# Optimization experiments

Hardware: AMD Instinct MI355X
Metric: run time of the kernel (lower is better)

The kernel has to match this reference:

```python
import jax, jax.numpy as jnp
import numpy as np

N_NODES = 50000
N_EDGES = 800000
D_IN = 128
D_OUT = 64


def setup_inputs() -> dict:
    key = jax.random.key(0)
    k_x, k_src, k_dst, k_val, k_w = jax.random.split(key, 5)
    x = jax.random.normal(k_x, (N_NODES, D_IN), dtype=jnp.float32)
    edge_src = jax.random.randint(k_src, (N_EDGES,), 0, N_NODES, dtype=jnp.int32)
    edge_dst = jnp.sort(jax.random.randint(k_dst, (N_EDGES,), 0, N_NODES, dtype=jnp.int32))
    edge_vals = jax.random.uniform(k_val, (N_EDGES,), dtype=jnp.float32)
    # Xavier-uniform init for weight, zeros for bias (matches reset_parameters)
    limit = float(np.sqrt(6.0 / (D_IN + D_OUT)))
    weight = jax.random.uniform(k_w, (D_IN, D_OUT), minval=-limit, maxval=limit, dtype=jnp.float32)
    bias = jnp.zeros((D_OUT,), dtype=jnp.float32)
    return {"x": x, "edge_src": edge_src, "edge_dst": edge_dst,
            "edge_vals": edge_vals, "weight": weight, "bias": bias}


def reference(x, edge_src, edge_dst, edge_vals, weight, bias):
    # Dense projection: [N, D_in] @ [D_in, D_out] -> [N, D_out]
    h = x @ weight
    # Sparse adjacency matmul (torch.spmm): out[i] = sum_{(j->i) in E} A_val * h[j]
    msgs = edge_vals[:, None] * h[edge_src]          # [E, D_out]
    agg = jax.ops.segment_sum(msgs, edge_dst, num_segments=N_NODES)  # [N, D_out]
    return agg + bias
```

## Files before the change

kernel.cpp:

```cpp
#include <hip/hip_runtime.h>

#define D_IN  128
#define D_OUT 64

__global__ __launch_bounds__(256, 4) void gemm_h_kernel(
    const float* __restrict__ x, const float* __restrict__ w,
    float* __restrict__ h, int n_nodes)
{
    __shared__ float Xs[64 * 132];
    __shared__ float Ws[128 * 64];

    const int t   = threadIdx.x;
    const int tx  = t & 15;
    const int ty  = t >> 4;
    const int node0 = blockIdx.x * 64;

    #pragma unroll
    for (int j = 0; j < 8; ++j) {
        int idx = j * 256 + t;
        int k   = idx >> 4;
        int c   = idx & 15;
        float4 v = *(const float4*)&w[k * D_OUT + c * 4];
        *(float4*)&Ws[k * 64 + c * 4] = v;
    }
    #pragma unroll
    for (int j = 0; j < 8; ++j) {
        int idx = j * 256 + t;
        int r   = idx >> 5;
        int c   = idx & 31;
        int gn  = node0 + r;
        float4 v = make_float4(0.f, 0.f, 0.f, 0.f);
        if (gn < n_nodes) v = *(const float4*)&x[(size_t)gn * D_IN + c * 4];
        *(float4*)&Xs[r * 132 + c * 4] = v;
    }
    __syncthreads();

    float4 acc[4];
    #pragma unroll
    for (int i = 0; i < 4; ++i) acc[i] = make_float4(0.f, 0.f, 0.f, 0.f);

    const int d0 = tx * 4;
    const int n0 = ty * 4;

    #pragma unroll 2
    for (int k = 0; k < D_IN; k += 4) {
        float4 xa[4], wb[4];
        #pragma unroll
        for (int i = 0; i < 4; ++i)
            xa[i] = *(const float4*)&Xs[(n0 + i) * 132 + k];
        #pragma unroll
        for (int r = 0; r < 4; ++r)
            wb[r] = *(const float4*)&Ws[(k + r) * 64 + d0];
        #pragma unroll
        for (int i = 0; i < 4; ++i) {
            acc[i].x = fmaf(xa[i].x, wb[0].x, acc[i].x);
            acc[i].y = fmaf(xa[i].x, wb[0].y, acc[i].y);
            acc[i].z = fmaf(xa[i].x, wb[0].z, acc[i].z);
            acc[i].w = fmaf(xa[i].x, wb[0].w, acc[i].w);
            acc[i].x = fmaf(xa[i].y, wb[1].x, acc[i].x);
            acc[i].y = fmaf(xa[i].y, wb[1].y, acc[i].y);
            acc[i].z = fmaf(xa[i].y, wb[1].z, acc[i].z);
            acc[i].w = fmaf(xa[i].y, wb[1].w, acc[i].w);
            acc[i].x = fmaf(xa[i].z, wb[2].x, acc[i].x);
            acc[i].y = fmaf(xa[i].z, wb[2].y, acc[i].y);
            acc[i].z = fmaf(xa[i].z, wb[2].z, acc[i].z);
            acc[i].w = fmaf(xa[i].z, wb[2].w, acc[i].w);
            acc[i].x = fmaf(xa[i].w, wb[3].x, acc[i].x);
            acc[i].y = fmaf(xa[i].w, wb[3].y, acc[i].y);
            acc[i].z = fmaf(xa[i].w, wb[3].z, acc[i].z);
            acc[i].w = fmaf(xa[i].w, wb[3].w, acc[i].w);
        }
    }

    #pragma unroll
    for (int i = 0; i < 4; ++i) {
        int gn = node0 + n0 + i;
        if (gn < n_nodes)
            *(float4*)&h[(size_t)gn * D_OUT + d0] = acc[i];
    }
}

__global__ __launch_bounds__(256) void build_row_ptr_kernel(
    const int* __restrict__ dst, int* __restrict__ row_ptr, int n_edges, int n_nodes)
{
    int e = blockIdx.x * blockDim.x + threadIdx.x;
    if (e >= n_edges) return;
    int d1 = dst[e];
    int d0 = (e == 0) ? -1 : dst[e - 1];
    for (int j = d0 + 1; j <= d1; ++j) row_ptr[j] = e;
    if (e == n_edges - 1) {
        for (int j = d1 + 1; j <= n_nodes; ++j) row_ptr[j] = n_edges;
    }
}

__global__ __launch_bounds__(256) void aggregate_kernel(
    const float4* __restrict__ h4, const int* __restrict__ src,
    const float* __restrict__ vals, const int* __restrict__ row_ptr,
    const float* __restrict__ bias, float* __restrict__ out, int n_nodes)
{
    int wave = (blockIdx.x * blockDim.x + threadIdx.x) >> 6;
    int lane = threadIdx.x & 63;
    if (wave >= n_nodes) return;
    int sub = lane >> 4;
    int d4  = lane & 15;

    int b = row_ptr[wave];
    int e = row_ptr[wave + 1];

    float4 acc = make_float4(0.f, 0.f, 0.f, 0.f);
    int k = b + sub;
    for (; k + 4 < e; k += 8) {
        int   s0 = src[k];     float v0 = vals[k];
        int   s1 = src[k + 4]; float v1 = vals[k + 4];
        float4 h0 = h4[(size_t)s0 * 16 + d4];
        float4 h1 = h4[(size_t)s1 * 16 + d4];
        acc.x = fmaf(v0, h0.x, acc.x);
        acc.y = fmaf(v0, h0.y, acc.y);
        acc.z = fmaf(v0, h0.z, acc.z);
        acc.w = fmaf(v0, h0.w, acc.w);
        acc.x = fmaf(v1, h1.x, acc.x);
        acc.y = fmaf(v1, h1.y, acc.y);
        acc.z = fmaf(v1, h1.z, acc.z);
        acc.w = fmaf(v1, h1.w, acc.w);
    }
    if (k < e) {
        int   s0 = src[k];
        float v0 = vals[k];
        float4 h0 = h4[(size_t)s0 * 16 + d4];
        acc.x = fmaf(v0, h0.x, acc.x);
        acc.y = fmaf(v0, h0.y, acc.y);
        acc.z = fmaf(v0, h0.z, acc.z);
        acc.w = fmaf(v0, h0.w, acc.w);
    }

    #pragma unroll
    for (int off = 16; off < 64; off <<= 1) {
        acc.x += __shfl_xor(acc.x, off, 64);
        acc.y += __shfl_xor(acc.y, off, 64);
        acc.z += __shfl_xor(acc.z, off, 64);
        acc.w += __shfl_xor(acc.w, off, 64);
    }

    if (sub == 0) {
        float4 bb = *(const float4*)&bias[d4 * 4];
        float4 o;
        o.x = acc.x + bb.x;
        o.y = acc.y + bb.y;
        o.z = acc.z + bb.z;
        o.w = acc.w + bb.w;
        *(float4*)&out[(size_t)wave * D_OUT + d4 * 4] = o;
    }
}

extern "C" void kernel_launch(void* const* d_in, const int* in_sizes, int n_in,
                              void* d_out, int out_size, void* d_ws, size_t ws_size,
                              hipStream_t stream)
{
    const float* x         = (const float*)d_in[0];
    const int*   edge_src  = (const int*)  d_in[1];
    const int*   edge_dst  = (const int*)  d_in[2];
    const float* edge_vals = (const float*)d_in[3];
    const float* weight    = (const float*)d_in[4];
    const float* bias      = (const float*)d_in[5];
    float*       out       = (float*)d_out;

    const int n_nodes = in_sizes[0] / D_IN;
    const int n_edges = in_sizes[1];

    float* h       = (float*)d_ws;
    int*   row_ptr = (int*)((char*)d_ws + (size_t)n_nodes * D_OUT * sizeof(float));

    {
        dim3 grid((n_nodes + 63) / 64), block(256);
        hipLaunchKernelGGL(gemm_h_kernel, grid, block, 0, stream, x, weight, h, n_nodes);
    }
    {
        dim3 grid((n_edges + 255) / 256), block(256);
        hipLaunchKernelGGL(build_row_ptr_kernel, grid, block, 0, stream,
                           edge_dst, row_ptr, n_edges, n_nodes);
    }
    {
        dim3 grid((n_nodes + 3) / 4), block(256);
        hipLaunchKernelGGL(aggregate_kernel, grid, block, 0, stream,
                           (const float4*)h, edge_src, edge_vals, row_ptr, bias, out, n_nodes);
    }
}
```

Baseline: 129.6 us.

## Merge row-pointer build into GEMM launch and deepen aggregation unroll

Folds the CSR row-pointer construction into the GEMM kernel as extra blocks in the same grid, removing one kernel launch and letting both independent jobs run concurrently. The aggregation loop is unrolled to 16 edges per iteration with two accumulators to keep more gathers in flight. The output is written with nontemporal stores. The extra blocks share the GEMM's large shared-memory footprint, which can limit their occupancy, and the wider unroll raises register use.

```diff
diff --git a/kernel.cpp b/kernel.cpp
--- a/kernel.cpp
+++ b/kernel.cpp
@@ -3,12 +3,34 @@
 #define D_IN  128
 #define D_OUT 64
 
-__global__ __launch_bounds__(256, 4) void gemm_h_kernel(
+typedef float nfloat4 __attribute__((ext_vector_type(4)));
+
+__global__ __launch_bounds__(256, 4) void gemm_rowptr_kernel(
     const float* __restrict__ x, const float* __restrict__ w,
-    float* __restrict__ h, int n_nodes)
+    float* __restrict__ h, int n_nodes,
+    const int* __restrict__ dst, int* __restrict__ row_ptr, int n_edges,
+    int gemm_blocks)
 {
     __shared__ float Xs[64 * 132];
     __shared__ float Ws[128 * 64];
+
+    if ((int)blockIdx.x >= gemm_blocks) {
+        int rb   = (int)blockIdx.x - gemm_blocks;
+        int base = rb * 1024 + (int)threadIdx.x;
+        #pragma unroll
+        for (int j = 0; j < 4; ++j) {
+            int e = base + j * 256;
+            if (e < n_edges) {
+                int d1 = dst[e];
+                int d0 = (e == 0) ? -1 : dst[e - 1];
+                for (int q = d0 + 1; q <= d1; ++q) row_ptr[q] = e;
+                if (e == n_edges - 1) {
+                    for (int q = d1 + 1; q <= n_nodes; ++q) row_ptr[q] = n_edges;
+                }
+            }
+        }
+        return;
+    }
 
     const int t   = threadIdx.x;
     const int tx  = t & 15;
@@ -80,19 +102,6 @@
     }
 }
 
-__global__ __launch_bounds__(256) void build_row_ptr_kernel(
-    const int* __restrict__ dst, int* __restrict__ row_ptr, int n_edges, int n_nodes)
-{
-    int e = blockIdx.x * blockDim.x + threadIdx.x;
-    if (e >= n_edges) return;
-    int d1 = dst[e];
-    int d0 = (e == 0) ? -1 : dst[e - 1];
-    for (int j = d0 + 1; j <= d1; ++j) row_ptr[j] = e;
-    if (e == n_edges - 1) {
-        for (int j = d1 + 1; j <= n_nodes; ++j) row_ptr[j] = n_edges;
-    }
-}
-
 __global__ __launch_bounds__(256) void aggregate_kernel(
     const float4* __restrict__ h4, const int* __restrict__ src,
     const float* __restrict__ vals, const int* __restrict__ row_ptr,
@@ -107,31 +116,67 @@
     int b = row_ptr[wave];
     int e = row_ptr[wave + 1];
 
-    float4 acc = make_float4(0.f, 0.f, 0.f, 0.f);
+    float4 bb = *(const float4*)&bias[d4 * 4];
+
+    float4 acc0 = make_float4(0.f, 0.f, 0.f, 0.f);
+    float4 acc1 = make_float4(0.f, 0.f, 0.f, 0.f);
+
     int k = b + sub;
+    for (; k + 12 < e; k += 16) {
+        int   s0 = src[k];      int   s1 = src[k + 4];
+        int   s2 = src[k + 8];  int   s3 = src[k + 12];
+        float v0 = vals[k];     float v1 = vals[k + 4];
+        float v2 = vals[k + 8]; float v3 = vals[k + 12];
+        float4 h0 = h4[(size_t)s0 * 16 + d4];
+        float4 h1 = h4[(size_t)s1 * 16 + d4];
+        float4 h2 = h4[(size_t)s2 * 16 + d4];
+        float4 h3 = h4[(size_t)s3 * 16 + d4];
+        acc0.x = fmaf(v0, h0.x, acc0.x);
+        acc0.y = fmaf(v0, h0.y, acc0.y);
+        acc0.z = fmaf(v0, h0.z, acc0.z);
+        acc0.w = fmaf(v0, h0.w, acc0.w);
+        acc1.x = fmaf(v1, h1.x, acc1.x);
+        acc1.y = fmaf(v1, h1.y, acc1.y);
+        acc1.z = fmaf(v1, h1.z, acc1.z);
+        acc1.w = fmaf(v1, h1.w, acc1.w);
+        acc0.x = fmaf(v2, h2.x, acc0.x);
+        acc0.y = fmaf(v2, h2.y, acc0.y);
+        acc0.z = fmaf(v2, h2.z, acc0.z);
+        acc0.w = fmaf(v2, h2.w, acc0.w);
+        acc1.x = fmaf(v3, h3.x, acc1.x);
+        acc1.y = fmaf(v3, h3.y, acc1.y);
+        acc1.z = fmaf(v3, h3.z, acc1.z);
+        acc1.w = fmaf(v3, h3.w, acc1.w);
+    }
     for (; k + 4 < e; k += 8) {
         int   s0 = src[k];     float v0 = vals[k];
         int   s1 = src[k + 4]; float v1 = vals[k + 4];
         float4 h0 = h4[(size_t)s0 * 16 + d4];
         float4 h1 = h4[(size_t)s1 * 16 + d4];
-        acc.x = fmaf(v0, h0.x, acc.x);
-        acc.y = fmaf(v0, h0.y, acc.y);
-        acc.z = fmaf(v0, h0.z, acc.z);
-        acc.w = fmaf(v0, h0.w, acc.w);
-        acc.x = fmaf(v1, h1.x, acc.x);
-        acc.y = fmaf(v1, h1.y, acc.y);
-        acc.z = fmaf(v1, h1.z, acc.z);
-        acc.w = fmaf(v1, h1.w, acc.w);
+        acc0.x = fmaf(v0, h0.x, acc0.x);
+        acc0.y = fmaf(v0, h0.y, acc0.y);
+        acc0.z = fmaf(v0, h0.z, acc0.z);
+        acc0.w = fmaf(v0, h0.w, acc0.w);
+        acc1.x = fmaf(v1, h1.x, acc1.x);
+        acc1.y = fmaf(v1, h1.y, acc1.y);
+        acc1.z = fmaf(v1, h1.z, acc1.z);
+        acc1.w = fmaf(v1, h1.w, acc1.w);
     }
     if (k < e) {
         int   s0 = src[k];
         float v0 = vals[k];
         float4 h0 = h4[(size_t)s0 * 16 + d4];
-        acc.x = fmaf(v0, h0.x, acc.x);
-        acc.y = fmaf(v0, h0.y, acc.y);
-        acc.z = fmaf(v0, h0.z, acc.z);
-        acc.w = fmaf(v0, h0.w, acc.w);
-    }
+        acc0.x = fmaf(v0, h0.x, acc0.x);
+        acc0.y = fmaf(v0, h0.y, acc0.y);
+        acc0.z = fmaf(v0, h0.z, acc0.z);
+        acc0.w = fmaf(v0, h0.w, acc0.w);
+    }
+
+    float4 acc;
+    acc.x = acc0.x + acc1.x;
+    acc.y = acc0.y + acc1.y;
+    acc.z = acc0.z + acc1.z;
+    acc.w = acc0.w + acc1.w;
 
     #pragma unroll
     for (int off = 16; off < 64; off <<= 1) {
@@ -142,13 +187,12 @@
     }
 
     if (sub == 0) {
-        float4 bb = *(const float4*)&bias[d4 * 4];
-        float4 o;
+        nfloat4 o;
         o.x = acc.x + bb.x;
         o.y = acc.y + bb.y;
         o.z = acc.z + bb.z;
         o.w = acc.w + bb.w;
-        *(float4*)&out[(size_t)wave * D_OUT + d4 * 4] = o;
+        __builtin_nontemporal_store(o, (nfloat4*)&out[(size_t)wave * D_OUT + d4 * 4]);
     }
 }
 
@@ -171,13 +215,12 @@
     int*   row_ptr = (int*)((char*)d_ws + (size_t)n_nodes * D_OUT * sizeof(float));
 
     {
-        dim3 grid((n_nodes + 63) / 64), block(256);
-        hipLaunchKernelGGL(gemm_h_kernel, grid, block, 0, stream, x, weight, h, n_nodes);
-    }
-    {
-        dim3 grid((n_edges + 255) / 256), block(256);
-        hipLaunchKernelGGL(build_row_ptr_kernel, grid, block, 0, stream,
-                           edge_dst, row_ptr, n_edges, n_nodes);
+        int gemm_blocks = (n_nodes + 63) / 64;
+        int rp_blocks   = (n_edges + 1023) / 1024;
+        dim3 grid(gemm_blocks + rp_blocks), block(256);
+        hipLaunchKernelGGL(gemm_rowptr_kernel, grid, block, 0, stream,
+                           x, weight, h, n_nodes,
+                           edge_dst, row_ptr, n_edges, gemm_blocks);
     }
     {
         dim3 grid((n_nodes + 3) / 4), block(256);
```

New measurement: 125.1 us. -3.4%, faster.
